# Optimization experiments

Hardware: AMD Instinct MI355X
Metric: run time of the kernel (lower is better)

## Reference

```python
import jax, jax.numpy as jnp
import numpy as np

B, N, E, H, T, FC = 16, 4096, 131072, 16, 3, 20


def setup_inputs() -> dict:
    key = jax.random.key(0)
    ks = jax.random.split(key, 16)
    F = jnp.eye(3, dtype=jnp.float32)[None] + 0.05 * jax.random.normal(ks[0], (B, 3, 3), dtype=jnp.float32)
    node_pos = jax.random.uniform(ks[1], (N, 3), dtype=jnp.float32)
    edge_src = jax.random.randint(ks[2], (E,), 0, N)
    edge_dst = jax.random.randint(ks[3], (E,), 0, N)
    edge_type = jax.random.randint(ks[4], (E,), 0, T)
    sc = lambda k, s: jax.random.normal(k, s, dtype=jnp.float32) / np.float32(np.sqrt(s[0]))
    return {
        'F': F, 'node_pos': node_pos,
        'edge_src': edge_src, 'edge_dst': edge_dst, 'edge_type': edge_type,
        'W_in': sc(ks[5], (3, H)),
        'fc1_0': sc(ks[6], (T, FC)), 'fc2_0': sc(ks[7], (FC, 1)), 'W_0': sc(ks[8], (H, H)),
        'fc1_1': sc(ks[9], (T, FC)), 'fc2_1': sc(ks[10], (FC, 1)), 'W_1': sc(ks[11], (H, H)),
        'W_out': sc(ks[12], (H, 3)),
        'w': jax.random.uniform(ks[13], (N * N,), dtype=jnp.float32),
    }


def _message_passing(Fx, edge_src, edge_dst, edge_oh,
                     W_in, fc1_0, fc2_0, W_0, fc1_1, fc2_1, W_1, W_out):
    # simplified stand-in for e3nn MessagePassing_v1: per-edge scalar gate from
    # edge-type MLP (fc_neurons=[3,20]), gather-scatter aggregation / sqrt(deg)
    inv_sqrt_deg = np.float32(1.0 / np.sqrt(edge_src.shape[0] / Fx.shape[1]))
    h = Fx @ W_in  # [B,N,H]
    for fc1, fc2, Wl in ((fc1_0, fc2_0, W_0), (fc1_1, fc2_1, W_1)):
        ew = jax.nn.relu(edge_oh @ fc1) @ fc2          # [E,1]
        msg = h[:, edge_src] * ew[None]                # [B,E,H]
        agg = jnp.zeros_like(h).at[:, edge_dst].add(msg) * inv_sqrt_deg
        h = jax.nn.relu(agg @ Wl)
    return h @ W_out  # [B,N,3]


def reference(F, node_pos, edge_src, edge_dst, edge_type,
              W_in, fc1_0, fc2_0, W_0, fc1_1, fc2_1, W_1, W_out, w):
    edge_oh = jax.nn.one_hot(edge_type, T, dtype=F.dtype)
    Fx = jnp.einsum('bij,nj->bni', F, node_pos)                     # deform positions
    h = _message_passing(Fx, edge_src, edge_dst, edge_oh,
                         W_in, fc1_0, fc2_0, W_0, fc1_1, fc2_1, W_1, W_out)
    Fx_ij = h[:, edge_src] - h[:, edge_dst]                         # [B,E,3]
    x_ij = jnp.einsum('bij,bej->bei', jnp.linalg.inv(F), Fx_ij)     # [B,E,3]
    n = node_pos.shape[0]
    a = Fx_ij[:, :n]  # original loop indexes first N edges with node index i
    c = x_ij[:, :n]
    W2 = w.reshape(n, n)
    # vectorized form of: sum_ij w[i*n+j] * kron(Fx_ij[b,i], x_ij[b,j])
    t = jnp.einsum('ij,bip->bjp', W2, a)                            # [B,N,3]
    stress = jnp.einsum('bjp,bjq->bpq', t, c).reshape(F.shape[0], 9)
    return stress
```

## Files before the change

kernel.cpp:

```cpp
#include <hip/hip_runtime.h>

#define N_NODES 4096
#define N_EDGES 131072
#define BATCH   16
#define HDIM    16
#define FCDIM   20
#define BH      256
#define ISD     0.17677669529663687f
#define NBSTRESS 2048

__device__ __forceinline__ float f4get(const float4& v, int k) {
    return k == 0 ? v.x : (k == 1 ? v.y : (k == 2 ? v.z : v.w));
}

template<int CTRL, int RM>
__device__ __forceinline__ float dpp_add(float v) {
    int sh = __builtin_amdgcn_update_dpp(0, __float_as_int(v), CTRL, RM, 0xF, true);
    return v + __int_as_float(sh);
}
__device__ __forceinline__ float wave_sum64(float v) {
    v = dpp_add<0xB1, 0xF>(v);
    v = dpp_add<0x4E, 0xF>(v);
    v = dpp_add<0x141,0xF>(v);
    v = dpp_add<0x140,0xF>(v);
    v = dpp_add<0x142,0xA>(v);
    v = dpp_add<0x143,0xC>(v);
    return v;
}

__global__ void setup_kernel(const float* __restrict__ F, const float* __restrict__ W_in,
                             const float* __restrict__ fc1_0, const float* __restrict__ fc2_0,
                             const float* __restrict__ fc1_1, const float* __restrict__ fc2_1,
                             float* __restrict__ ew, float* __restrict__ G,
                             float* __restrict__ invF, float* __restrict__ out144,
                             int* __restrict__ cnt) {
    int t = threadIdx.x;
    if (t < 6) {
        const float* fc1 = (t < 3) ? fc1_0 : fc1_1;
        const float* fc2 = (t < 3) ? fc2_0 : fc2_1;
        int ty = t % 3;
        float s = 0.f;
        for (int f = 0; f < FCDIM; ++f) {
            float v = fc1[ty * FCDIM + f];
            v = v > 0.f ? v : 0.f;
            s += v * fc2[f];
        }
        ew[t] = s;
    }
    for (int idx = t; idx < BATCH * 3 * HDIM; idx += 256) {
        int b = idx / 48, r = idx % 48, j = r / HDIM, k = r % HDIM;
        float s = 0.f;
        for (int i = 0; i < 3; ++i) s += F[b * 9 + i * 3 + j] * W_in[i * HDIM + k];
        G[idx] = s;
    }
    if (t < BATCH) {
        const float* f = F + t * 9;
        float a00=f[0],a01=f[1],a02=f[2],a10=f[3],a11=f[4],a12=f[5],a20=f[6],a21=f[7],a22=f[8];
        float det = a00*(a11*a22-a12*a21) - a01*(a10*a22-a12*a20) + a02*(a10*a21-a11*a20);
        float id = 1.f/det;
        float* o = invF + t*9;
        o[0]=(a11*a22-a12*a21)*id; o[1]=(a02*a21-a01*a22)*id; o[2]=(a01*a12-a02*a11)*id;
        o[3]=(a12*a20-a10*a22)*id; o[4]=(a00*a22-a02*a20)*id; o[5]=(a02*a10-a00*a12)*id;
        o[6]=(a10*a21-a11*a20)*id; o[7]=(a01*a20-a00*a21)*id; o[8]=(a00*a11-a01*a10)*id;
    }
    if (t < 144) out144[t] = 0.f;
    for (int i = t; i < N_NODES; i += 256) cnt[i] = 0;
}

__global__ void h0_hist_kernel(const float* __restrict__ pos, const float* __restrict__ G,
                               float* __restrict__ h0,
                               const int* __restrict__ edst, int* __restrict__ cnt) {
    int bid = blockIdx.x;
    int t = threadIdx.x;
    if (bid < 1024) {
        int id = bid * 256 + t;
        int n  = id >> 6;
        int c4 = (id & 63) << 2;
        int b  = c4 >> 4;
        int k  = c4 & 15;
        float p0 = pos[n*3+0], p1 = pos[n*3+1], p2 = pos[n*3+2];
        const float* g = G + b*48 + k;
        float4 r;
        r.x = p0*g[0] + p1*g[16] + p2*g[32];
        r.y = p0*g[1] + p1*g[17] + p2*g[33];
        r.z = p0*g[2] + p1*g[18] + p2*g[34];
        r.w = p0*g[3] + p1*g[19] + p2*g[35];
        *(float4*)(h0 + n*BH + c4) = r;
    } else {
        int e = (bid - 1024) * 256 + t;
        if (e < N_EDGES) atomicAdd(&cnt[edst[e]], 1);
    }
}

__global__ void scan_kernel(const int* __restrict__ cnt, int* __restrict__ off,
                            int* __restrict__ cursor) {
    __shared__ int wsum[4];
    int t = threadIdx.x;
    int lane = t & 63, wave = t >> 6;
    int base = t * 16;
    int loc[16];
    int s = 0;
    #pragma unroll
    for (int i = 0; i < 16; ++i) { loc[i] = s; s += cnt[base + i]; }
    int pre = s;
    #pragma unroll
    for (int o = 1; o < 64; o <<= 1) {
        int v = __shfl_up(pre, o);
        if (lane >= o) pre += v;
    }
    if (lane == 63) wsum[wave] = pre;
    __syncthreads();
    int woff = 0;
    #pragma unroll
    for (int w = 0; w < 4; ++w) if (w < wave) woff += wsum[w];
    int excl = woff + pre - s;
    #pragma unroll
    for (int i = 0; i < 16; ++i) {
        int v = excl + loc[i];
        off[base + i] = v;
        cursor[base + i] = v;
    }
    if (t == 255) off[N_NODES] = excl + s;
}
__global__ void fill_kernel(const int* __restrict__ src, const int* __restrict__ dst,
                            const int* __restrict__ typ, int* __restrict__ cursor,
                            int* __restrict__ sedge) {
    int e = blockIdx.x * 256 + threadIdx.x;
    if (e < N_EDGES) {
        int p = atomicAdd(&cursor[dst[e]], 1);
        sedge[p] = src[e] | (typ[e] << 16);
    }
}

__global__ void layer_kernel(const float* __restrict__ h_in, float* __restrict__ h_out,
                             const int* __restrict__ off, const int* __restrict__ sedge,
                             const float* __restrict__ ew3, const float* __restrict__ W) {
    __shared__ float Wl[256];
    __shared__ float aggS[2][16*17 + 4];
    int t = threadIdx.x;
    Wl[t] = W[t];
    int wave = t >> 6, lane = t & 63;
    int node = wave >> 1;
    int half = wave & 1;
    int d = blockIdx.x * 2 + node;
    float e0 = ew3[0], e1 = ew3[1], e2 = ew3[2];
    int beg = off[d], end = off[d+1];
    int col = half * 128 + lane * 2;
    float2 acc = {0.f, 0.f};
    int it = beg;
    for (; it + 7 < end; it += 8) {
        int v[8]; float2 hv[8];
        #pragma unroll
        for (int u = 0; u < 8; ++u) v[u] = sedge[it + u];
        #pragma unroll
        for (int u = 0; u < 8; ++u)
            hv[u] = *(const float2*)(h_in + (v[u] & 0xFFFF) * BH + col);
        #pragma unroll
        for (int u = 0; u < 8; ++u) {
            int ty = v[u] >> 16;
            float wg = (ty == 0) ? e0 : (ty == 1 ? e1 : e2);
            acc.x += wg * hv[u].x; acc.y += wg * hv[u].y;
        }
    }
    for (; it < end; ++it) {
        int v = sedge[it];
        int ty = v >> 16;
        float wg = (ty == 0) ? e0 : (ty == 1 ? e1 : e2);
        float2 hv = *(const float2*)(h_in + (v & 0xFFFF) * BH + col);
        acc.x += wg * hv.x; acc.y += wg * hv.y;
    }
    int b = col >> 4, k0 = col & 15;
    aggS[node][b*17 + k0]     = acc.x * ISD;
    aggS[node][b*17 + k0 + 1] = acc.y * ISD;
    __syncthreads();
    int en = t >> 7, c2 = (t & 127) * 2;
    int eb = c2 >> 4, ek = c2 & 15;
    const float* arow = aggS[en] + eb * 17;
    float o0 = 0.f, o1 = 0.f;
    #pragma unroll
    for (int k = 0; k < 16; ++k) {
        float av = arow[k];
        o0 += av * Wl[k*16 + ek];
        o1 += av * Wl[k*16 + ek + 1];
    }
    int ed = blockIdx.x * 2 + en;
    float2 r;
    r.x = o0 > 0.f ? o0 : 0.f;
    r.y = o1 > 0.f ? o1 : 0.f;
    *(float2*)(h_out + ed*BH + c2) = r;
}

__global__ void hout_kernel(const float* __restrict__ h2, const float* __restrict__ Wout,
                            float* __restrict__ hout) {
    __shared__ float Wo[48];
    int t = threadIdx.x;
    if (t < 48) Wo[t] = Wout[t];
    __syncthreads();
    int id = blockIdx.x * 256 + t;
    int n = id >> 4, b = id & 15;
    const float* hr = h2 + n*BH + b*HDIM;
    float s0=0.f, s1=0.f, s2=0.f;
    #pragma unroll
    for (int k = 0; k < 16; ++k) {
        float v = hr[k];
        s0 += v*Wo[k*3+0]; s1 += v*Wo[k*3+1]; s2 += v*Wo[k*3+2];
    }
    float* o = hout + n*48 + b*3;
    o[0]=s0; o[1]=s1; o[2]=s2;
}

__global__ void ac_kernel(const float* __restrict__ hout, const int* __restrict__ esrc,
                          const int* __restrict__ edst, const float* __restrict__ invF,
                          float* __restrict__ a, float* __restrict__ c) {
    __shared__ float iF[144];
    int t = threadIdx.x;
    if (t < 144) iF[t] = invF[t];
    __syncthreads();
    int id = blockIdx.x * 256 + t;
    int i = id >> 4, b = id & 15;
    int s = esrc[i], d = edst[i];
    float a0 = hout[s*48+b*3+0] - hout[d*48+b*3+0];
    float a1 = hout[s*48+b*3+1] - hout[d*48+b*3+1];
    float a2 = hout[s*48+b*3+2] - hout[d*48+b*3+2];
    float* ap = a + i*48 + b*3;
    ap[0]=a0; ap[1]=a1; ap[2]=a2;
    const float* m = iF + b*9;
    float* cp = c + i*48 + b*3;
    cp[0] = m[0]*a0 + m[1]*a1 + m[2]*a2;
    cp[1] = m[3]*a0 + m[4]*a1 + m[5]*a2;
    cp[2] = m[6]*a0 + m[7]*a1 + m[8]*a2;
}

__global__ __launch_bounds__(256, 6)
void stress_fused_kernel(const float* __restrict__ W2, const float* __restrict__ a,
                         const float* __restrict__ c, float* __restrict__ P) {
    __shared__ float sa[64 * 48];
    int t = threadIdx.x;
    int lane = t & 63;
    int wave = t >> 6;
    int cg   = wave * 12;
    int jb    = (blockIdx.x & 31) * 128;
    int strip = blockIdx.x >> 5;
    int i0    = strip * 64;
    {
        const float4* ga = (const float4*)(a + (size_t)i0 * 48);
        float4* la = (float4*)sa;
        #pragma unroll
        for (int k = 0; k < 3; ++k) la[t + k * 256] = ga[t + k * 256];
    }
    __syncthreads();
    int j = jb + lane * 2;
    const float* w2p = W2 + (size_t)i0 * N_NODES + j;
    float4 acc[2][3];
    #pragma unroll
    for (int jj = 0; jj < 2; ++jj)
        #pragma unroll
        for (int q = 0; q < 3; ++q) acc[jj][q] = make_float4(0.f,0.f,0.f,0.f);
    float2 w[8];
    #pragma unroll
    for (int u = 0; u < 8; ++u)
        w[u] = *(const float2*)(w2p + (size_t)u * N_NODES);
    #pragma unroll 1
    for (int base = 0; base < 64; base += 8) {
        float2 wn[8];
        #pragma unroll
        for (int u = 0; u < 8; ++u) {
            int r = base + 8 + u; if (r > 63) r = 63;
            wn[u] = *(const float2*)(w2p + (size_t)r * N_NODES);
        }
        #pragma unroll
        for (int u = 0; u < 8; ++u) {
            const float* ar = &sa[(base + u) * 48 + cg];
            float4 x = *(const float4*)(ar);
            float4 y = *(const float4*)(ar + 4);
            float4 z = *(const float4*)(ar + 8);
            #pragma unroll
            for (int jj = 0; jj < 2; ++jj) {
                float wv = jj == 0 ? w[u].x : w[u].y;
                acc[jj][0].x += wv*x.x; acc[jj][0].y += wv*x.y;
                acc[jj][0].z += wv*x.z; acc[jj][0].w += wv*x.w;
                acc[jj][1].x += wv*y.x; acc[jj][1].y += wv*y.y;
                acc[jj][1].z += wv*y.z; acc[jj][1].w += wv*y.w;
                acc[jj][2].x += wv*z.x; acc[jj][2].y += wv*z.y;
                acc[jj][2].z += wv*z.z; acc[jj][2].w += wv*z.w;
            }
        }
        #pragma unroll
        for (int u = 0; u < 8; ++u) w[u] = wn[u];
    }
    float s[36];
    #pragma unroll
    for (int m = 0; m < 36; ++m) s[m] = 0.f;
    #pragma unroll
    for (int jj = 0; jj < 2; ++jj) {
        const float* cvp = c + (size_t)(jb + lane * 2 + jj) * 48 + cg;
        float4 c0 = *(const float4*)(cvp);
        float4 c1 = *(const float4*)(cvp + 4);
        float4 c2 = *(const float4*)(cvp + 8);
        float cv[12] = {c0.x,c0.y,c0.z,c0.w, c1.x,c1.y,c1.z,c1.w, c2.x,c2.y,c2.z,c2.w};
        #pragma unroll
        for (int cc = 0; cc < 12; ++cc) {
            float tv = f4get(acc[jj][cc >> 2], cc & 3);
            int qb = (cc / 3) * 3;
            s[cc*3+0] += tv * cv[qb+0];
            s[cc*3+1] += tv * cv[qb+1];
            s[cc*3+2] += tv * cv[qb+2];
        }
    }
    #pragma unroll
    for (int m = 0; m < 36; ++m) s[m] = wave_sum64(s[m]);
    if (lane == 63) {
        #pragma unroll
        for (int m = 0; m < 36; ++m) {
            int cc = m / 3, q = m % 3;
            int bp = cg + cc;
            P[(size_t)((bp / 3) * 9 + (bp % 3) * 3 + q) * NBSTRESS + blockIdx.x] = s[m];
        }
    }
}

__global__ void stress_reduce_kernel(const float* __restrict__ P, float* __restrict__ out) {
    __shared__ float wsum[4];
    int t = threadIdx.x, lane = t & 63, wave = t >> 6;
    const float* p = P + (size_t)blockIdx.x * NBSTRESS;
    float4 v0 = *(const float4*)(p + t * 8);
    float4 v1 = *(const float4*)(p + t * 8 + 4);
    float s = v0.x+v0.y+v0.z+v0.w + v1.x+v1.y+v1.z+v1.w;
    #pragma unroll
    for (int o = 1; o < 64; o <<= 1) s += __shfl_xor(s, o);
    if (lane == 0) wsum[wave] = s;
    __syncthreads();
    if (t == 0) out[blockIdx.x] = wsum[0] + wsum[1] + wsum[2] + wsum[3];
}

extern "C" void kernel_launch(void* const* d_in, const int* in_sizes, int n_in,
                              void* d_out, int out_size, void* d_ws, size_t ws_size,
                              hipStream_t stream) {
    const float* F     = (const float*)d_in[0];
    const float* pos   = (const float*)d_in[1];
    const int*   esrc  = (const int*)d_in[2];
    const int*   edst  = (const int*)d_in[3];
    const int*   etyp  = (const int*)d_in[4];
    const float* W_in  = (const float*)d_in[5];
    const float* fc1_0 = (const float*)d_in[6];
    const float* fc2_0 = (const float*)d_in[7];
    const float* W_0   = (const float*)d_in[8];
    const float* fc1_1 = (const float*)d_in[9];
    const float* fc2_1 = (const float*)d_in[10];
    const float* W_1   = (const float*)d_in[11];
    const float* W_out = (const float*)d_in[12];
    const float* w2    = (const float*)d_in[13];
    float* out = (float*)d_out;

    float* ws   = (float*)d_ws;
    float* ew   = ws;
    float* G    = ws + 16;
    float* invF = ws + 800;
    float* bufA = ws + 1024;
    float* bufB = bufA + N_NODES*BH;
    float* hout = bufB + N_NODES*BH;
    float* aArr = hout + N_NODES*48;
    float* cArr = aArr + N_NODES*48;
    int* cnt    = (int*)(cArr + N_NODES*48);
    int* off    = cnt + N_NODES;
    int* cursor = off + N_NODES + 1;
    int* sedge  = cursor + N_NODES;
    float* P    = (float*)(sedge + N_EDGES);

    setup_kernel<<<1, 256, 0, stream>>>(F, W_in, fc1_0, fc2_0, fc1_1, fc2_1, ew, G, invF, out, cnt);
    h0_hist_kernel<<<1536, 256, 0, stream>>>(pos, G, bufA, edst, cnt);
    scan_kernel<<<1, 256, 0, stream>>>(cnt, off, cursor);
    fill_kernel<<<512, 256, 0, stream>>>(esrc, edst, etyp, cursor, sedge);
    layer_kernel<<<2048, 256, 0, stream>>>(bufA, bufB, off, sedge, ew,     W_0);
    layer_kernel<<<2048, 256, 0, stream>>>(bufB, bufA, off, sedge, ew + 3, W_1);
    hout_kernel<<<256, 256, 0, stream>>>(bufA, W_out, hout);
    ac_kernel<<<256, 256, 0, stream>>>(hout, esrc, edst, invF, aArr, cArr);
    stress_fused_kernel<<<NBSTRESS, 256, 0, stream>>>(w2, aArr, cArr, P);
    stress_reduce_kernel<<<144, 256, 0, stream>>>(P, out);
}
```

Baseline: 213.4 us.

## Fuse output projection into edge-diff kernel and widen stress tile per lane

Removes the separate hout kernel by applying W_out inside ac_kernel on the difference of the source and destination hidden rows, which drops one launch and one intermediate buffer. The stress kernel now has each lane handle 4 columns of W2 using float4 loads, and the block count is halved to 1024 with a matching change to the partial-sum reduction. The shared-memory staging of a is dropped in favour of wave-uniform global loads. The larger per-thread accumulator raises register pressure, and the launch bound drops to 4 blocks per CU, so latency hiding may suffer.

Measured after the change: 223.0 us. 1.04x slower.

```diff
diff --git a/kernel.cpp b/kernel.cpp
--- a/kernel.cpp
+++ b/kernel.cpp
@@ -7,7 +7,7 @@
 #define FCDIM   20
 #define BH      256
 #define ISD     0.17677669529663687f
-#define NBSTRESS 2048
+#define NBSTRESS 1024
 
 __device__ __forceinline__ float f4get(const float4& v, int k) {
     return k == 0 ? v.x : (k == 1 ? v.y : (k == 2 ? v.z : v.w));
@@ -190,38 +190,27 @@
     *(float2*)(h_out + ed*BH + c2) = r;
 }
 
-__global__ void hout_kernel(const float* __restrict__ h2, const float* __restrict__ Wout,
-                            float* __restrict__ hout) {
-    __shared__ float Wo[48];
-    int t = threadIdx.x;
-    if (t < 48) Wo[t] = Wout[t];
-    __syncthreads();
-    int id = blockIdx.x * 256 + t;
-    int n = id >> 4, b = id & 15;
-    const float* hr = h2 + n*BH + b*HDIM;
-    float s0=0.f, s1=0.f, s2=0.f;
-    #pragma unroll
-    for (int k = 0; k < 16; ++k) {
-        float v = hr[k];
-        s0 += v*Wo[k*3+0]; s1 += v*Wo[k*3+1]; s2 += v*Wo[k*3+2];
-    }
-    float* o = hout + n*48 + b*3;
-    o[0]=s0; o[1]=s1; o[2]=s2;
-}
-
-__global__ void ac_kernel(const float* __restrict__ hout, const int* __restrict__ esrc,
-                          const int* __restrict__ edst, const float* __restrict__ invF,
+__global__ void ac_kernel(const float* __restrict__ h2, const float* __restrict__ Wout,
+                          const int* __restrict__ esrc, const int* __restrict__ edst,
+                          const float* __restrict__ invF,
                           float* __restrict__ a, float* __restrict__ c) {
     __shared__ float iF[144];
+    __shared__ float Wo[48];
     int t = threadIdx.x;
     if (t < 144) iF[t] = invF[t];
+    else if (t < 192) Wo[t - 144] = Wout[t - 144];
     __syncthreads();
     int id = blockIdx.x * 256 + t;
     int i = id >> 4, b = id & 15;
     int s = esrc[i], d = edst[i];
-    float a0 = hout[s*48+b*3+0] - hout[d*48+b*3+0];
-    float a1 = hout[s*48+b*3+1] - hout[d*48+b*3+1];
-    float a2 = hout[s*48+b*3+2] - hout[d*48+b*3+2];
+    const float* hs = h2 + s*BH + b*HDIM;
+    const float* hd = h2 + d*BH + b*HDIM;
+    float a0 = 0.f, a1 = 0.f, a2 = 0.f;
+    #pragma unroll
+    for (int k = 0; k < 16; ++k) {
+        float dv = hs[k] - hd[k];
+        a0 += dv*Wo[k*3+0]; a1 += dv*Wo[k*3+1]; a2 += dv*Wo[k*3+2];
+    }
     float* ap = a + i*48 + b*3;
     ap[0]=a0; ap[1]=a1; ap[2]=a2;
     const float* m = iF + b*9;
@@ -231,52 +220,45 @@
     cp[2] = m[6]*a0 + m[7]*a1 + m[8]*a2;
 }
 
-__global__ __launch_bounds__(256, 6)
+__global__ __launch_bounds__(256, 4)
 void stress_fused_kernel(const float* __restrict__ W2, const float* __restrict__ a,
                          const float* __restrict__ c, float* __restrict__ P) {
-    __shared__ float sa[64 * 48];
     int t = threadIdx.x;
     int lane = t & 63;
     int wave = t >> 6;
-    int cg   = wave * 12;
-    int jb    = (blockIdx.x & 31) * 128;
-    int strip = blockIdx.x >> 5;
+    int cg   = __builtin_amdgcn_readfirstlane(wave * 12);
+    int jb    = (blockIdx.x & 15) * 256;
+    int strip = blockIdx.x >> 4;
     int i0    = strip * 64;
-    {
-        const float4* ga = (const float4*)(a + (size_t)i0 * 48);
-        float4* la = (float4*)sa;
-        #pragma unroll
-        for (int k = 0; k < 3; ++k) la[t + k * 256] = ga[t + k * 256];
-    }
-    __syncthreads();
-    int j = jb + lane * 2;
+    int j = jb + lane * 4;
     const float* w2p = W2 + (size_t)i0 * N_NODES + j;
-    float4 acc[2][3];
-    #pragma unroll
-    for (int jj = 0; jj < 2; ++jj)
+    const float* ap  = a + (size_t)i0 * 48 + cg;
+    float4 acc[4][3];
+    #pragma unroll
+    for (int jj = 0; jj < 4; ++jj)
         #pragma unroll
         for (int q = 0; q < 3; ++q) acc[jj][q] = make_float4(0.f,0.f,0.f,0.f);
-    float2 w[8];
-    #pragma unroll
-    for (int u = 0; u < 8; ++u)
-        w[u] = *(const float2*)(w2p + (size_t)u * N_NODES);
+    float4 w[4];
+    #pragma unroll
+    for (int u = 0; u < 4; ++u)
+        w[u] = *(const float4*)(w2p + (size_t)u * N_NODES);
     #pragma unroll 1
-    for (int base = 0; base < 64; base += 8) {
-        float2 wn[8];
-        #pragma unroll
-        for (int u = 0; u < 8; ++u) {
-            int r = base + 8 + u; if (r > 63) r = 63;
-            wn[u] = *(const float2*)(w2p + (size_t)r * N_NODES);
-        }
-        #pragma unroll
-        for (int u = 0; u < 8; ++u) {
-            const float* ar = &sa[(base + u) * 48 + cg];
+    for (int base = 0; base < 64; base += 4) {
+        float4 wn[4];
+        #pragma unroll
+        for (int u = 0; u < 4; ++u) {
+            int r = base + 4 + u; if (r > 63) r = 63;
+            wn[u] = *(const float4*)(w2p + (size_t)r * N_NODES);
+        }
+        #pragma unroll
+        for (int u = 0; u < 4; ++u) {
+            const float* ar = ap + (size_t)(base + u) * 48;
             float4 x = *(const float4*)(ar);
             float4 y = *(const float4*)(ar + 4);
             float4 z = *(const float4*)(ar + 8);
             #pragma unroll
-            for (int jj = 0; jj < 2; ++jj) {
-                float wv = jj == 0 ? w[u].x : w[u].y;
+            for (int jj = 0; jj < 4; ++jj) {
+                float wv = f4get(w[u], jj);
                 acc[jj][0].x += wv*x.x; acc[jj][0].y += wv*x.y;
                 acc[jj][0].z += wv*x.z; acc[jj][0].w += wv*x.w;
                 acc[jj][1].x += wv*y.x; acc[jj][1].y += wv*y.y;
@@ -286,14 +268,14 @@
             }
         }
         #pragma unroll
-        for (int u = 0; u < 8; ++u) w[u] = wn[u];
+        for (int u = 0; u < 4; ++u) w[u] = wn[u];
     }
     float s[36];
     #pragma unroll
     for (int m = 0; m < 36; ++m) s[m] = 0.f;
     #pragma unroll
-    for (int jj = 0; jj < 2; ++jj) {
-        const float* cvp = c + (size_t)(jb + lane * 2 + jj) * 48 + cg;
+    for (int jj = 0; jj < 4; ++jj) {
+        const float* cvp = c + (size_t)(jb + lane * 4 + jj) * 48 + cg;
         float4 c0 = *(const float4*)(cvp);
         float4 c1 = *(const float4*)(cvp + 4);
         float4 c2 = *(const float4*)(cvp + 8);
@@ -323,9 +305,8 @@
     __shared__ float wsum[4];
     int t = threadIdx.x, lane = t & 63, wave = t >> 6;
     const float* p = P + (size_t)blockIdx.x * NBSTRESS;
-    float4 v0 = *(const float4*)(p + t * 8);
-    float4 v1 = *(const float4*)(p + t * 8 + 4);
-    float s = v0.x+v0.y+v0.z+v0.w + v1.x+v1.y+v1.z+v1.w;
+    float4 v = *(const float4*)(p + t * 4);
+    float s = v.x + v.y + v.z + v.w;
     #pragma unroll
     for (int o = 1; o < 64; o <<= 1) s += __shfl_xor(s, o);
     if (lane == 0) wsum[wave] = s;
@@ -358,8 +339,7 @@
     float* invF = ws + 800;
     float* bufA = ws + 1024;
     float* bufB = bufA + N_NODES*BH;
-    float* hout = bufB + N_NODES*BH;
-    float* aArr = hout + N_NODES*48;
+    float* aArr = bufB + N_NODES*BH;
     float* cArr = aArr + N_NODES*48;
     int* cnt    = (int*)(cArr + N_NODES*48);
     int* off    = cnt + N_NODES;
@@ -373,8 +353,7 @@
     fill_kernel<<<512, 256, 0, stream>>>(esrc, edst, etyp, cursor, sedge);
     layer_kernel<<<2048, 256, 0, stream>>>(bufA, bufB, off, sedge, ew,     W_0);
     layer_kernel<<<2048, 256, 0, stream>>>(bufB, bufA, off, sedge, ew + 3, W_1);
-    hout_kernel<<<256, 256, 0, stream>>>(bufA, W_out, hout);
-    ac_kernel<<<256, 256, 0, stream>>>(hout, esrc, edst, invF, aArr, cArr);
+    ac_kernel<<<256, 256, 0, stream>>>(bufA, W_out, esrc, edst, invF, aArr, cArr);
     stress_fused_kernel<<<NBSTRESS, 256, 0, stream>>>(w2, aArr, cArr, P);
     stress_reduce_kernel<<<144, 256, 0, stream>>>(P, out);
 }
```
